# Kernel tuning notes

Measured on AMD Instinct MI355X. Metric: run time of the kernel, lower is better.

Reference implementation:

```python
import jax, jax.numpy as jnp
import numpy as np

N_QUBITS = 16
N_LAYERS = 3
N_STATES = 2 ** N_QUBITS


def setup_inputs() -> dict:
    key = jax.random.key(0)
    ks = jax.random.split(key, 6)
    B = 256
    return {
        "molecular_features": jax.random.normal(ks[0], (B, 100), jnp.float32),
        "rotation_params": jax.random.normal(ks[1], (N_LAYERS, N_QUBITS, 3), jnp.float32),
        "entangling_params": jax.random.normal(ks[2], (N_LAYERS, N_QUBITS - 1), jnp.float32),
        "W1": jax.random.normal(ks[3], (100, 64), jnp.float32) * 0.1,
        "b1": jnp.zeros((64,), jnp.float32),
        "W2": jax.random.normal(ks[4], (64, N_QUBITS), jnp.float32) * 0.1,
        "b2": jnp.zeros((N_QUBITS,), jnp.float32),
    }


def _apply_single_qubit(amp, q, M):
    # bit q occupies the 2^q place in the flat index -> reshape so it is its own axis
    B = amp.shape[0]
    a = amp.reshape(B, -1, 2, 2 ** q)  # (B, high, bit_q, low)
    out = jnp.einsum('bij,bhjl->bhil', M, a)
    return out.reshape(B, N_STATES)


def _apply_cnot(amp, control, target, p):
    # torch per-state loop is equivalent (reads come from OLD amplitudes, pair
    # written twice with identical symmetric values) to:
    #   new[s] = (1-p)*old[s] + p*old[s ^ (1<<target)]   if control bit of s is 1
    #   new[s] = old[s]                                  otherwise
    B = amp.shape[0]
    a = amp.reshape(B, -1, 2, 2 ** target)
    flipped = jnp.flip(a, axis=2).reshape(B, N_STATES)
    ctrl = ((jnp.arange(N_STATES) >> control) & 1).astype(bool)
    mixed = (1.0 - p) * amp + p * flipped
    return jnp.where(ctrl[None, :], mixed, amp)


def _forward(molecular_features, rotation_params, entangling_params, W1, b1, W2, b2):
    h = jnp.tanh(jax.nn.relu(molecular_features @ W1 + b1) @ W2 + b2)  # (B, n_qubits)
    B = molecular_features.shape[0]
    amp = jnp.zeros((B, N_STATES), jnp.complex64).at[:, 0].set(1.0)
    for layer in range(N_LAYERS):
        for q in range(N_QUBITS):
            ang = rotation_params[layer, q][None, :] * h[:, q][:, None]  # (B, 3)
            c = jnp.cos(0.5 * ang)
            s = jnp.sin(0.5 * ang)
            cx, cy, cz = c[:, 0], c[:, 1], c[:, 2]
            sx, sy, sz = s[:, 0], s[:, 1], s[:, 2]
            # matches the (non-unitary) torch rotation_matrix construction
            M = jnp.stack(
                [cx * cy * cz, -sx * sy * sz, sx * sy * cz, cx * cy * sz], axis=-1
            ).reshape(B, 2, 2).astype(jnp.complex64)
            amp = _apply_single_qubit(amp, q, M)
        for q in range(N_QUBITS - 1):
            p = jax.nn.sigmoid(entangling_params[layer, q])
            amp = _apply_cnot(amp, q, q + 1, p)
    return amp


def reference(molecular_features, rotation_params, entangling_params, W1, b1, W2, b2):
    return _forward(molecular_features, rotation_params, entangling_params, W1, b1, W2, b2)
```

## Files before the change

kernel.cpp:

```cpp
#include <hip/hip_runtime.h>
#include <math.h>

#define NQ 16
#define NLAYERS 3
#define NSTATES 65536
#define BATCH 256

__device__ __forceinline__ float rd(const float* __restrict__ p, int i, int n) {
    return p[i < n ? i : (n - 1)];
}

template <int I> struct IC { static constexpr int v = I; };

template <int I, int N, typename F>
__device__ __forceinline__ void sfor_i(F& f) {
    if constexpr (I < N) {
        f(IC<I>{});
        sfor_i<I + 1, N>(f);
    }
}
template <int N, typename F>
__device__ __forceinline__ void sfor(F&& f) { sfor_i<0, N>(f); }

__device__ __forceinline__ void mix2(float& a, float& b, float p) {
    float na = (1.f - p) * a + p * b;
    float nb = (1.f - p) * b + p * a;
    a = na; b = nb;
}
__device__ __forceinline__ void mixc(float& a, float& b, float qc, float pc) {
    float na = qc * a + pc * b;
    float nb = qc * b + pc * a;
    a = na; b = nb;
}
__device__ __forceinline__ void bf2(float& a0, float& a1, float4 m) {
    float n0 = m.x * a0 + m.y * a1;
    float n1 = m.z * a0 + m.w * a1;
    a0 = n0; a1 = n1;
}

__device__ __forceinline__ int ladr(int row, int col) {
    return row * 1025 + col;
}

__global__
__attribute__((amdgpu_flat_work_group_size(1024, 1024)))
void qsim(const float* __restrict__ x,
          const float* __restrict__ rot,
          const float* __restrict__ ent,
          const float* __restrict__ W1,
          const float* __restrict__ b1,
          const float* __restrict__ W2,
          const float* __restrict__ b2,
          float* __restrict__ out,
          long long out_floats,
          int nx, int nrot, int nent, int nW1, int nb1, int nW2, int nb2) {
    const int tid  = threadIdx.x;
    const int b    = blockIdx.x;
    const int lane = tid & 63;
    const int wave = tid >> 6;
    const int wq   = (tid >> 8) & 3;
    const int wv   = (tid >> 6) & 3;

    __shared__ float  ldsS[32 * 1025];
    __shared__ float  scr[4 * 1024];
    __shared__ float4 Mg[NLAYERS * NQ];
    __shared__ float  pg[NLAYERS * (NQ - 1)];
    __shared__ float  hidS[64];
    __shared__ float  hqS[16];

    if (tid < 64) {
        float s = rd(b1, tid, nb1);
        for (int k = 0; k < 100; k++)
            s = fmaf(rd(x, b * 100 + k, nx), rd(W1, k * 64 + tid, nW1), s);
        hidS[tid] = fmaxf(s, 0.f);
    } else if (tid >= 64 && tid < 64 + NLAYERS * (NQ - 1)) {
        int i = tid - 64;
        pg[i] = 1.f / (1.f + expf(-rd(ent, i, nent)));
    }
    __syncthreads();

    if (tid < 16) {
        float s = rd(b2, tid, nb2);
#pragma unroll
        for (int i = 0; i < 64; i++)
            s = fmaf(hidS[i], rd(W2, i * 16 + tid, nW2), s);
        hqS[tid] = tanhf(s);
    }
    __syncthreads();

    if (tid < NLAYERS * NQ) {
        int q = tid & 15;
        float hv = hqS[q];
        float a0 = 0.5f * rd(rot, tid * 3 + 0, nrot) * hv;
        float a1 = 0.5f * rd(rot, tid * 3 + 1, nrot) * hv;
        float a2 = 0.5f * rd(rot, tid * 3 + 2, nrot) * hv;
        float cx = cosf(a0), sx = sinf(a0);
        float cy = cosf(a1), sy = sinf(a1);
        float cz = cosf(a2), sz = sinf(a2);
        Mg[tid] = make_float4(cx * cy * cz, -(sx * sy * sz),
                              sx * sy * cz,  cx * cy * sz);
    }
    __syncthreads();

    float r[32];
    sfor<32>([&](auto J) { r[J.v] = 0.f; });
    if (tid == 0) r[0] = 1.f;

    for (int l = 0; l < NLAYERS; l++) {
        if (l > 0) {
            float p13p = pg[(l - 1) * 15 + 13];
            float p14p = pg[(l - 1) * 15 + 14];
            sfor<8>([&](auto K) { mix2(r[8 + K.v], r[24 + K.v], p13p); });
            float4 m13 = Mg[l * NQ + 13];
            float4 m14 = Mg[l * NQ + 14];
            sfor<8>([&](auto W) {
                float t0 = ldsS[ladr(W.v,      tid)];
                float t1 = ldsS[ladr(W.v + 8,  tid)];
                float t2 = ldsS[ladr(W.v + 16, tid)];
                float t3 = ldsS[ladr(W.v + 24, tid)];
                mix2(t1, t3, p13p);
                mix2(r[W.v + 16], t2, p14p);
                mix2(r[W.v + 24], t3, p14p);
                bf2(t0, t1, m13); bf2(t2, t3, m13);
                bf2(t0, t2, m14); bf2(t1, t3, m14);
                ldsS[ladr(W.v,      tid)] = t0;
                ldsS[ladr(W.v + 8,  tid)] = t1;
                ldsS[ladr(W.v + 16, tid)] = t2;
                ldsS[ladr(W.v + 24, tid)] = t3;
            });
            sfor<8>([&](auto K) { bf2(r[K.v],      r[K.v + 8],  m13); });
            sfor<8>([&](auto K) { bf2(r[K.v + 16], r[K.v + 24], m13); });
            sfor<16>([&](auto K) { bf2(r[K.v], r[K.v + 16], m14); });
            sfor<4>([&](auto W) {
                float t[8];
                sfor<8>([&](auto K) { t[K.v] = ldsS[ladr(W.v * 8 + K.v, tid)]; });
                sfor<3>([&](auto QQ) {
                    float4 m = Mg[l * NQ + 10 + QQ.v];
                    sfor<8>([&](auto K) {
                        constexpr int h = 1 << QQ.v;
                        if constexpr (!(K.v & h)) bf2(t[K.v], t[K.v | h], m);
                    });
                });
                sfor<8>([&](auto K) { ldsS[ladr(W.v * 8 + K.v, tid)] = t[K.v]; });
            });
            sfor<3>([&](auto QQ) {
                float4 m = Mg[l * NQ + 10 + QQ.v];
                sfor<32>([&](auto J) {
                    constexpr int h = 1 << QQ.v;
                    if constexpr (!(J.v & h)) bf2(r[J.v], r[J.v | h], m);
                });
            });
        } else {
            sfor<5>([&](auto QQ) {
                float4 m = Mg[10 + QQ.v];
                sfor<32>([&](auto J) {
                    constexpr int h = 1 << QQ.v;
                    if constexpr (!(J.v & h)) bf2(r[J.v], r[J.v | h], m);
                });
            });
        }

#pragma unroll
        for (int q = 0; q < 6; q++) {
            float4 m = Mg[l * NQ + q];
            int bit = (tid >> q) & 1;
            float cown  = bit ? m.w : m.x;
            float cpart = bit ? m.z : m.y;
            sfor<4>([&](auto C) {
                sfor<8>([&](auto K) {
                    constexpr int j = C.v * 8 + K.v;
                    float part = __shfl_xor(r[j], 1 << q);
                    r[j] = cown * r[j] + cpart * part;
                });
                __builtin_amdgcn_sched_barrier(0);
            });
        }
#pragma unroll
        for (int c = 0; c < 5; c++) {
            float p = pg[l * 15 + c];
            int ctl = (tid >> c) & 1;
            float pc = ctl ? p : 0.f;
            float qc = ctl ? (1.f - p) : 1.f;
            sfor<4>([&](auto C) {
                sfor<8>([&](auto K) {
                    constexpr int j = C.v * 8 + K.v;
                    float f = __shfl_xor(r[j], 1 << (c + 1));
                    r[j] = qc * r[j] + pc * f;
                });
                __builtin_amdgcn_sched_barrier(0);
            });
        }

        if (l > 0) {
            __syncthreads();
            const int Rlow  = tid & 15;
            const int Cbase = tid & 0x3F0;
            const int bit4  = (tid >> 4) & 1;
            const int bit5  = (tid >> 5) & 1;
            sfor<2>([&](auto H) {
                const int R    = H.v * 16 + Rlow;
                const int base = ladr(R, Cbase);
                float v[16];
                sfor<16>([&](auto J) { v[J.v] = ldsS[base + J.v]; });
                sfor<4>([&](auto Q) {
                    float4 m = Mg[l * NQ + Q.v];
                    sfor<16>([&](auto J) {
                        constexpr int h = 1 << Q.v;
                        if constexpr (!(J.v & h)) bf2(v[J.v], v[J.v | h], m);
                    });
                });
                {
                    float4 m = Mg[l * NQ + 4];
                    float cown  = bit4 ? m.w : m.x;
                    float cpart = bit4 ? m.z : m.y;
                    sfor<2>([&](auto C) {
                        sfor<8>([&](auto K) {
                            constexpr int j = C.v * 8 + K.v;
                            float part = __shfl_xor(v[j], 16);
                            v[j] = cown * v[j] + cpart * part;
                        });
                        __builtin_amdgcn_sched_barrier(0);
                    });
                }
                {
                    float4 m = Mg[l * NQ + 5];
                    float cown  = bit5 ? m.w : m.x;
                    float cpart = bit5 ? m.z : m.y;
                    sfor<2>([&](auto C) {
                        sfor<8>([&](auto K) {
                            constexpr int j = C.v * 8 + K.v;
                            float part = __shfl_xor(v[j], 32);
                            v[j] = cown * v[j] + cpart * part;
                        });
                        __builtin_amdgcn_sched_barrier(0);
                    });
                }
                {
                    float p = pg[l * 15 + 0];
                    sfor<16>([&](auto J) {
                        if constexpr ((J.v & 1) && !(J.v & 2)) mix2(v[J.v], v[J.v | 2], p);
                    });
                }
                {
                    float p = pg[l * 15 + 1];
                    sfor<16>([&](auto J) {
                        if constexpr ((J.v & 2) && !(J.v & 4)) mix2(v[J.v], v[J.v | 4], p);
                    });
                }
                {
                    float p = pg[l * 15 + 2];
                    sfor<16>([&](auto J) {
                        if constexpr ((J.v & 4) && !(J.v & 8)) mix2(v[J.v], v[J.v | 8], p);
                    });
                }
                {
                    float p = pg[l * 15 + 3];
                    sfor<8>([&](auto K) {
                        constexpr int j = 8 + K.v;
                        float f = __shfl_xor(v[j], 16);
                        v[j] = (1.f - p) * v[j] + p * f;
                    });
                    __builtin_amdgcn_sched_barrier(0);
                }
                {
                    float p = pg[l * 15 + 4];
                    float pc = bit4 ? p : 0.f;
                    float qc = bit4 ? (1.f - p) : 1.f;
                    sfor<2>([&](auto C) {
                        sfor<8>([&](auto K) {
                            constexpr int j = C.v * 8 + K.v;
                            float f = __shfl_xor(v[j], 32);
                            v[j] = qc * v[j] + pc * f;
                        });
                        __builtin_amdgcn_sched_barrier(0);
                    });
                }
                sfor<16>([&](auto J) { ldsS[base + J.v] = v[J.v]; });
            });
        }

        {
            float p5 = pg[l * 15 + 5];
            int ctl5 = (tid >> 5) & 1;
            float pc5 = ctl5 ? p5 : 0.f;
            float qc5 = ctl5 ? (1.f - p5) : 1.f;
            sfor<2>([&](auto B14) {
                float val[16];
                sfor<4>([&](auto J) {
                    sfor<4>([&](auto V) {
                        scr[V.v * 1024 + tid] = r[B14.v * 16 + J.v * 4 + V.v];
                    });
                    __syncthreads();
                    if (wq == J.v) {
                        sfor<16>([&](auto G) { val[G.v] = scr[wv * 1024 + G.v * 64 + lane]; });
                    }
                    __syncthreads();
                });
                sfor<4>([&](auto Q) {
                    float4 m = Mg[l * NQ + 6 + Q.v];
                    sfor<16>([&](auto G) {
                        constexpr int h = 1 << Q.v;
                        if constexpr (!(G.v & h)) bf2(val[G.v], val[G.v | h], m);
                    });
                });
                sfor<16>([&](auto G) {
                    if constexpr (!(G.v & 1)) mixc(val[G.v], val[G.v | 1], qc5, pc5);
                });
                sfor<3>([&](auto CC) {
                    float p = pg[l * 15 + 6 + CC.v];
                    sfor<16>([&](auto G) {
                        constexpr int cm = 1 << CC.v;
                        constexpr int tm = 2 << CC.v;
                        if constexpr ((G.v & cm) && !(G.v & tm))
                            mix2(val[G.v], val[G.v | tm], p);
                    });
                });
                sfor<16>([&](auto G) { r[B14.v * 16 + G.v] = val[G.v]; });

                float vL[16];
                if (l > 0) {
                    const int srow = B14.v * 16 + wave;
                    const int base = ladr(srow, lane);
                    sfor<16>([&](auto G) { vL[G.v] = ldsS[base + G.v * 64]; });
                    sfor<4>([&](auto Q) {
                        float4 m = Mg[l * NQ + 6 + Q.v];
                        sfor<16>([&](auto G) {
                            constexpr int h = 1 << Q.v;
                            if constexpr (!(G.v & h)) bf2(vL[G.v], vL[G.v | h], m);
                        });
                    });
                    sfor<16>([&](auto G) {
                        if constexpr (!(G.v & 1)) mixc(vL[G.v], vL[G.v | 1], qc5, pc5);
                    });
                    sfor<3>([&](auto CC) {
                        float p = pg[l * 15 + 6 + CC.v];
                        sfor<16>([&](auto G) {
                            constexpr int cm = 1 << CC.v;
                            constexpr int tm = 2 << CC.v;
                            if constexpr ((G.v & cm) && !(G.v & tm))
                                mix2(vL[G.v], vL[G.v | tm], p);
                        });
                    });
                } else {
                    sfor<16>([&](auto G) { vL[G.v] = 0.f; });
                }
                {
                    float4 m15 = Mg[l * NQ + 15];
                    sfor<16>([&](auto G) { bf2(r[B14.v * 16 + G.v], vL[G.v], m15); });
                }
                __syncthreads();
                sfor<16>([&](auto G) { ldsS[ladr(B14.v * 16 + G.v, tid)] = vL[G.v]; });
            });
        }

        {
            float p9 = pg[l * 15 + 9];
            int ctl9 = (tid >> 9) & 1;
            float pc9 = ctl9 ? p9 : 0.f;
            float qc9 = ctl9 ? (1.f - p9) : 1.f;
            sfor<2>([&](auto B14) {
                float val[16];
                sfor<4>([&](auto J) {
                    sfor<4>([&](auto V) {
                        scr[V.v * 1024 + tid] = r[B14.v * 16 + J.v * 4 + V.v];
                    });
                    __syncthreads();
                    if (wq == J.v) {
                        sfor<16>([&](auto H) { val[H.v] = scr[wv * 1024 + H.v * 64 + lane]; });
                    }
                    __syncthreads();
                });
                sfor<16>([&](auto H) {
                    if constexpr (!(H.v & 1)) mixc(val[H.v], val[H.v | 1], qc9, pc9);
                });
                sfor<3>([&](auto CC) {
                    float p = pg[l * 15 + 10 + CC.v];
                    sfor<16>([&](auto H) {
                        constexpr int cm = 1 << CC.v;
                        constexpr int tm = 2 << CC.v;
                        if constexpr ((H.v & cm) && !(H.v & tm))
                            mix2(val[H.v], val[H.v | tm], p);
                    });
                });
                sfor<16>([&](auto H) { r[B14.v * 16 + H.v] = val[H.v]; });

                float vL[16];
                {
                    const int srow = B14.v * 16 + wave;
                    const int base = ladr(srow, lane);
                    sfor<16>([&](auto H) { vL[H.v] = ldsS[base + H.v * 64]; });
                }
                sfor<16>([&](auto H) {
                    if constexpr (!(H.v & 1)) mixc(vL[H.v], vL[H.v | 1], qc9, pc9);
                });
                sfor<3>([&](auto CC) {
                    float p = pg[l * 15 + 10 + CC.v];
                    sfor<16>([&](auto H) {
                        constexpr int cm = 1 << CC.v;
                        constexpr int tm = 2 << CC.v;
                        if constexpr ((H.v & cm) && !(H.v & tm))
                            mix2(vL[H.v], vL[H.v | tm], p);
                    });
                });
                __syncthreads();
                sfor<16>([&](auto H) { ldsS[ladr(B14.v * 16 + H.v, tid)] = vL[H.v]; });
            });
            __syncthreads();
        }
    }

    {
        float p13 = pg[2 * 15 + 13];
        float p14 = pg[2 * 15 + 14];
        sfor<8>([&](auto K) { mix2(r[8 + K.v], r[24 + K.v], p13); });
        long long base = (long long)b * NSTATES;
        sfor<8>([&](auto W) {
            float t0 = ldsS[ladr(W.v,      tid)];
            float t1 = ldsS[ladr(W.v + 8,  tid)];
            float t2 = ldsS[ladr(W.v + 16, tid)];
            float t3 = ldsS[ladr(W.v + 24, tid)];
            mix2(t1, t3, p13);
            mix2(r[W.v + 16], t2, p14);
            mix2(r[W.v + 24], t3, p14);
            long long fb = base + 32768LL + (long long)(W.v * 1024) + tid;
            if (fb             < out_floats) out[fb]             = t0;
            if (fb + 8  * 1024 < out_floats) out[fb + 8  * 1024] = t1;
            if (fb + 16 * 1024 < out_floats) out[fb + 16 * 1024] = t2;
            if (fb + 24 * 1024 < out_floats) out[fb + 24 * 1024] = t3;
        });
        sfor<32>([&](auto J) {
            long long fi = base + (long long)(J.v * 1024) + tid;
            if (fi < out_floats) out[fi] = r[J.v];
        });
    }
}

extern "C" void kernel_launch(void* const* d_in, const int* in_sizes, int n_in,
                              void* d_out, int out_size, void* d_ws, size_t ws_size,
                              hipStream_t stream) {
    const float* x   = (const float*)d_in[0];
    const float* rot = (const float*)d_in[1];
    const float* ent = (const float*)d_in[2];
    const float* W1  = (const float*)d_in[3];
    const float* b1  = (const float*)d_in[4];
    const float* W2  = (const float*)d_in[5];
    const float* b2  = (const float*)d_in[6];

    qsim<<<BATCH, 1024, 0, stream>>>(x, rot, ent, W1, b1, W2, b2,
                                     (float*)d_out, (long long)out_size,
                                     in_sizes[0], in_sizes[1], in_sizes[2],
                                     in_sizes[3], in_sizes[4], in_sizes[5],
                                     in_sizes[6]);
}
```

Baseline: 216.6 us.

## Move qubit 10-13 rotations into transposed phase and shrink shuffle batches

Rotations for qubits 10-13 no longer run in the register-resident prologue. They now run in the transposed phase just before the qubit-9 controlled mixes, where those bits are register-local, so the extra passes over the whole state are dropped. Shuffle batches are cut from 8 to 4 per scheduling barrier, likely to lower register pressure. Four registers are spilled to scratch around the LDS phase. Extra sched barriers after the LDS loads add ordering constraints, and the changed gate order must still match the reference.

```diff
diff --git a/kernel.cpp b/kernel.cpp
--- a/kernel.cpp
+++ b/kernel.cpp
@@ -110,54 +110,28 @@
         if (l > 0) {
             float p13p = pg[(l - 1) * 15 + 13];
             float p14p = pg[(l - 1) * 15 + 14];
-            sfor<8>([&](auto K) { mix2(r[8 + K.v], r[24 + K.v], p13p); });
-            float4 m13 = Mg[l * NQ + 13];
             float4 m14 = Mg[l * NQ + 14];
             sfor<8>([&](auto W) {
                 float t0 = ldsS[ladr(W.v,      tid)];
                 float t1 = ldsS[ladr(W.v + 8,  tid)];
                 float t2 = ldsS[ladr(W.v + 16, tid)];
                 float t3 = ldsS[ladr(W.v + 24, tid)];
+                mix2(r[8 + W.v], r[24 + W.v], p13p);
                 mix2(t1, t3, p13p);
-                mix2(r[W.v + 16], t2, p14p);
-                mix2(r[W.v + 24], t3, p14p);
-                bf2(t0, t1, m13); bf2(t2, t3, m13);
-                bf2(t0, t2, m14); bf2(t1, t3, m14);
+                mix2(r[16 + W.v], t2, p14p);
+                mix2(r[24 + W.v], t3, p14p);
+                bf2(r[W.v], r[16 + W.v], m14);
+                bf2(r[8 + W.v], r[24 + W.v], m14);
+                bf2(t0, t2, m14);
+                bf2(t1, t3, m14);
                 ldsS[ladr(W.v,      tid)] = t0;
                 ldsS[ladr(W.v + 8,  tid)] = t1;
                 ldsS[ladr(W.v + 16, tid)] = t2;
                 ldsS[ladr(W.v + 24, tid)] = t3;
             });
-            sfor<8>([&](auto K) { bf2(r[K.v],      r[K.v + 8],  m13); });
-            sfor<8>([&](auto K) { bf2(r[K.v + 16], r[K.v + 24], m13); });
+        } else {
+            float4 m14 = Mg[14];
             sfor<16>([&](auto K) { bf2(r[K.v], r[K.v + 16], m14); });
-            sfor<4>([&](auto W) {
-                float t[8];
-                sfor<8>([&](auto K) { t[K.v] = ldsS[ladr(W.v * 8 + K.v, tid)]; });
-                sfor<3>([&](auto QQ) {
-                    float4 m = Mg[l * NQ + 10 + QQ.v];
-                    sfor<8>([&](auto K) {
-                        constexpr int h = 1 << QQ.v;
-                        if constexpr (!(K.v & h)) bf2(t[K.v], t[K.v | h], m);
-                    });
-                });
-                sfor<8>([&](auto K) { ldsS[ladr(W.v * 8 + K.v, tid)] = t[K.v]; });
-            });
-            sfor<3>([&](auto QQ) {
-                float4 m = Mg[l * NQ + 10 + QQ.v];
-                sfor<32>([&](auto J) {
-                    constexpr int h = 1 << QQ.v;
-                    if constexpr (!(J.v & h)) bf2(r[J.v], r[J.v | h], m);
-                });
-            });
-        } else {
-            sfor<5>([&](auto QQ) {
-                float4 m = Mg[10 + QQ.v];
-                sfor<32>([&](auto J) {
-                    constexpr int h = 1 << QQ.v;
-                    if constexpr (!(J.v & h)) bf2(r[J.v], r[J.v | h], m);
-                });
-            });
         }
 
 #pragma unroll
@@ -166,9 +140,9 @@
             int bit = (tid >> q) & 1;
             float cown  = bit ? m.w : m.x;
             float cpart = bit ? m.z : m.y;
-            sfor<4>([&](auto C) {
-                sfor<8>([&](auto K) {
-                    constexpr int j = C.v * 8 + K.v;
+            sfor<8>([&](auto C) {
+                sfor<4>([&](auto K) {
+                    constexpr int j = C.v * 4 + K.v;
                     float part = __shfl_xor(r[j], 1 << q);
                     r[j] = cown * r[j] + cpart * part;
                 });
@@ -181,9 +155,9 @@
             int ctl = (tid >> c) & 1;
             float pc = ctl ? p : 0.f;
             float qc = ctl ? (1.f - p) : 1.f;
-            sfor<4>([&](auto C) {
-                sfor<8>([&](auto K) {
-                    constexpr int j = C.v * 8 + K.v;
+            sfor<8>([&](auto C) {
+                sfor<4>([&](auto K) {
+                    constexpr int j = C.v * 4 + K.v;
                     float f = __shfl_xor(r[j], 1 << (c + 1));
                     r[j] = qc * r[j] + pc * f;
                 });
@@ -192,6 +166,7 @@
         }
 
         if (l > 0) {
+            sfor<4>([&](auto V) { scr[V.v * 1024 + tid] = r[28 + V.v]; });
             __syncthreads();
             const int Rlow  = tid & 15;
             const int Cbase = tid & 0x3F0;
@@ -213,9 +188,9 @@
                     float4 m = Mg[l * NQ + 4];
                     float cown  = bit4 ? m.w : m.x;
                     float cpart = bit4 ? m.z : m.y;
-                    sfor<2>([&](auto C) {
-                        sfor<8>([&](auto K) {
-                            constexpr int j = C.v * 8 + K.v;
+                    sfor<4>([&](auto C) {
+                        sfor<4>([&](auto K) {
+                            constexpr int j = C.v * 4 + K.v;
                             float part = __shfl_xor(v[j], 16);
                             v[j] = cown * v[j] + cpart * part;
                         });
@@ -226,9 +201,9 @@
                     float4 m = Mg[l * NQ + 5];
                     float cown  = bit5 ? m.w : m.x;
                     float cpart = bit5 ? m.z : m.y;
-                    sfor<2>([&](auto C) {
-                        sfor<8>([&](auto K) {
-                            constexpr int j = C.v * 8 + K.v;
+                    sfor<4>([&](auto C) {
+                        sfor<4>([&](auto K) {
+                            constexpr int j = C.v * 4 + K.v;
                             float part = __shfl_xor(v[j], 32);
                             v[j] = cown * v[j] + cpart * part;
                         });
@@ -255,20 +230,22 @@
                 }
                 {
                     float p = pg[l * 15 + 3];
-                    sfor<8>([&](auto K) {
-                        constexpr int j = 8 + K.v;
-                        float f = __shfl_xor(v[j], 16);
-                        v[j] = (1.f - p) * v[j] + p * f;
-                    });
-                    __builtin_amdgcn_sched_barrier(0);
+                    sfor<2>([&](auto C) {
+                        sfor<4>([&](auto K) {
+                            constexpr int j = 8 + C.v * 4 + K.v;
+                            float f = __shfl_xor(v[j], 16);
+                            v[j] = (1.f - p) * v[j] + p * f;
+                        });
+                        __builtin_amdgcn_sched_barrier(0);
+                    });
                 }
                 {
                     float p = pg[l * 15 + 4];
                     float pc = bit4 ? p : 0.f;
                     float qc = bit4 ? (1.f - p) : 1.f;
-                    sfor<2>([&](auto C) {
-                        sfor<8>([&](auto K) {
-                            constexpr int j = C.v * 8 + K.v;
+                    sfor<4>([&](auto C) {
+                        sfor<4>([&](auto K) {
+                            constexpr int j = C.v * 4 + K.v;
                             float f = __shfl_xor(v[j], 32);
                             v[j] = qc * v[j] + pc * f;
                         });
@@ -277,6 +254,7 @@
                 }
                 sfor<16>([&](auto J) { ldsS[base + J.v] = v[J.v]; });
             });
+            sfor<4>([&](auto V) { r[28 + V.v] = scr[V.v * 1024 + tid]; });
         }
 
         {
@@ -322,6 +300,7 @@
                     const int srow = B14.v * 16 + wave;
                     const int base = ladr(srow, lane);
                     sfor<16>([&](auto G) { vL[G.v] = ldsS[base + G.v * 64]; });
+                    __builtin_amdgcn_sched_barrier(0);
                     sfor<4>([&](auto Q) {
                         float4 m = Mg[l * NQ + 6 + Q.v];
                         sfor<16>([&](auto G) {
@@ -370,6 +349,13 @@
                     }
                     __syncthreads();
                 });
+                sfor<4>([&](auto QQ) {
+                    float4 m = Mg[l * NQ + 10 + QQ.v];
+                    sfor<16>([&](auto H) {
+                        constexpr int h = 1 << QQ.v;
+                        if constexpr (!(H.v & h)) bf2(val[H.v], val[H.v | h], m);
+                    });
+                });
                 sfor<16>([&](auto H) {
                     if constexpr (!(H.v & 1)) mixc(val[H.v], val[H.v | 1], qc9, pc9);
                 });
@@ -389,7 +375,15 @@
                     const int srow = B14.v * 16 + wave;
                     const int base = ladr(srow, lane);
                     sfor<16>([&](auto H) { vL[H.v] = ldsS[base + H.v * 64]; });
-                }
+                    __builtin_amdgcn_sched_barrier(0);
+                }
+                sfor<4>([&](auto QQ) {
+                    float4 m = Mg[l * NQ + 10 + QQ.v];
+                    sfor<16>([&](auto H) {
+                        constexpr int h = 1 << QQ.v;
+                        if constexpr (!(H.v & h)) bf2(vL[H.v], vL[H.v | h], m);
+                    });
+                });
                 sfor<16>([&](auto H) {
                     if constexpr (!(H.v & 1)) mixc(vL[H.v], vL[H.v | 1], qc9, pc9);
                 });
```

Measured after the change: 214.9 us. No clear change (-0.8%).
